# Kernel tuning notes

Measured on AMD Instinct MI355X. Metric: run time of the kernel, lower is better.

The kernel has to match this reference:

```python
import jax, jax.numpy as jnp
import numpy as np

ALPHA = 1.0

def setup_inputs() -> dict:
    key = jax.random.key(0)
    kz, kc = jax.random.split(key)
    N, K, D = 65536, 256, 256
    z = jax.random.normal(kz, (N, D), dtype=jnp.float32)
    centroids = jax.random.normal(kc, (K, D), dtype=jnp.float32)
    return {"z": z, "centroids": centroids}

def reference(z, centroids):
    # squared euclidean distances (N, K) via expansion; same math as
    # sum((z[:,None,:]-c)**2, -1) without the (N,K,D) intermediate
    z2 = jnp.sum(z * z, axis=1, keepdims=True)            # (N, 1)
    c2 = jnp.sum(centroids * centroids, axis=1)           # (K,)
    sse = jnp.maximum(z2 + c2[None, :] - 2.0 * (z @ centroids.T), 0.0)
    # Student-t kernel
    q = (1.0 + sse / ALPHA) ** (-(ALPHA + 1.0) / 2.0)
    q = q / jnp.sum(q, axis=1, keepdims=True)             # row normalize
    # target distribution p
    sf = q * q / jnp.sum(q, axis=0, keepdims=True)        # col normalize of q^2
    p = sf / jnp.sum(sf, axis=1, keepdims=True)           # row normalize
    return (p, q)
```

## Files before the change

kernel.cpp:

```cpp
#include <hip/hip_runtime.h>
#include <stdint.h>

#define N_ROWS 65536
#define K_CENT 256
#define D_DIM  256

typedef __attribute__((ext_vector_type(8))) short bf16x8;
typedef __attribute__((ext_vector_type(4))) float f32x4;

__device__ __forceinline__ float bf2f(unsigned short u) {
    union { unsigned int i; float f; } v;
    v.i = ((unsigned int)u) << 16;
    return v.f;
}

__device__ __forceinline__ unsigned short f2bf(float f) {
    union { float f; unsigned int i; } v;
    v.f = f;
    unsigned int r = (v.i + 0x7FFFu + ((v.i >> 16) & 1u)) >> 16;
    return (unsigned short)r;
}

__global__ void c2_kernel(const float* __restrict__ cent,
                          float* __restrict__ c2,
                          unsigned short* __restrict__ cent_bf) {
    int row  = blockIdx.x;
    int lane = threadIdx.x;
    const float4 v = *(const float4*)(cent + (size_t)row * D_DIM + lane * 4);
    unsigned short b0 = f2bf(v.x), b1 = f2bf(v.y), b2 = f2bf(v.z), b3 = f2bf(v.w);
    ushort4 bv; bv.x = b0; bv.y = b1; bv.z = b2; bv.w = b3;
    int blk = lane >> 1;
    int pos = row * D_DIM + (((blk ^ (row & 7)) << 3) | ((lane & 1) << 2));
    *(ushort4*)(cent_bf + pos) = bv;
    float f0 = bf2f(b0), f1 = bf2f(b1), f2 = bf2f(b2), f3 = bf2f(b3);
    float s = f0 * f0 + f1 * f1 + f2 * f2 + f3 * f3;
    #pragma unroll
    for (int off = 32; off >= 1; off >>= 1) s += __shfl_xor(s, off, 64);
    if (lane == 0) c2[row] = s;
}

__global__ __launch_bounds__(256, 3) void pass1_kernel(
        const float* __restrict__ z,
        const unsigned short* __restrict__ cent_bf,
        const float* __restrict__ c2,
        float* __restrict__ partials,
        float* __restrict__ q_out) {
    __shared__ __align__(16) unsigned short bstage[64 * D_DIM];
    __shared__ float col_lds[4][K_CENT];

    const int tid  = threadIdx.x;
    const int wave = tid >> 6;
    const int lane = tid & 63;
    const int m15  = lane & 15;
    const int quad = lane >> 4;
    const int row0 = blockIdx.x * 64 + wave * 16;

    const float* za = z + (size_t)(row0 + m15) * D_DIM + quad * 8;
    bf16x8 afrag[8];
    float z2p = 0.0f;
    #pragma unroll
    for (int h = 0; h < 2; ++h) {
        float4 a[8];
        #pragma unroll
        for (int i = 0; i < 4; ++i) {
            a[2 * i]     = *(const float4*)(za + h * 128 + i * 32);
            a[2 * i + 1] = *(const float4*)(za + h * 128 + i * 32 + 4);
        }
        #pragma unroll
        for (int i = 0; i < 4; ++i) {
            const int ks = h * 4 + i;
            const float av[8] = {a[2*i].x, a[2*i].y, a[2*i].z, a[2*i].w,
                                 a[2*i+1].x, a[2*i+1].y, a[2*i+1].z, a[2*i+1].w};
            #pragma unroll
            for (int j = 0; j < 8; ++j) {
                unsigned short ub = f2bf(av[j]);
                afrag[ks][j] = (short)ub;
                float f = bf2f(ub);
                z2p += f * f;
            }
        }
    }
    z2p += __shfl_xor(z2p, 16, 64);
    z2p += __shfl_xor(z2p, 32, 64);
    float z2r[4];
    #pragma unroll
    for (int r = 0; r < 4; ++r) z2r[r] = __shfl(z2p, quad * 4 + r, 64);

    f32x4 acc[16];
    #pragma unroll
    for (int t = 0; t < 16; ++t) acc[t] = (f32x4){0.f, 0.f, 0.f, 0.f};

    #pragma unroll
    for (int c = 0; c < 4; ++c) {
        const unsigned short* src = cent_bf + (size_t)c * 64 * D_DIM;
        bf16x8 st[8];
        #pragma unroll
        for (int i = 0; i < 8; ++i)
            st[i] = *(const bf16x8*)&src[(i * 256 + tid) * 8];
        #pragma unroll
        for (int i = 0; i < 8; ++i)
            *(bf16x8*)&bstage[(i * 256 + tid) * 8] = st[i];
        __syncthreads();
        #pragma unroll
        for (int ks = 0; ks < 8; ++ks) {
            #pragma unroll
            for (int t = 0; t < 4; ++t) {
                int r_local = t * 16 + m15;
                int b = quad + ks * 4;
                int pos = r_local * D_DIM + ((b ^ (r_local & 7)) << 3);
                bf16x8 bfrag = *(const bf16x8*)&bstage[pos];
                acc[c * 4 + t] = __builtin_amdgcn_mfma_f32_16x16x32_bf16(
                    afrag[ks], bfrag, acc[c * 4 + t], 0, 0, 0);
            }
        }
        __syncthreads();
    }

    float rowsum[4] = {0.f, 0.f, 0.f, 0.f};
    #pragma unroll
    for (int t = 0; t < 16; ++t) {
        float c2v = c2[t * 16 + m15];
        #pragma unroll
        for (int r = 0; r < 4; ++r) {
            float sse = z2r[r] + c2v - 2.0f * acc[t][r];
            sse = fmaxf(sse, 0.0f);
            float u = 1.0f / (1.0f + sse);
            acc[t][r] = u;
            rowsum[r] += u;
        }
    }
    #pragma unroll
    for (int r = 0; r < 4; ++r) {
        float v = rowsum[r];
        v += __shfl_xor(v, 1, 64);
        v += __shfl_xor(v, 2, 64);
        v += __shfl_xor(v, 4, 64);
        v += __shfl_xor(v, 8, 64);
        rowsum[r] = 1.0f / v;
    }

    float colp[16];
    #pragma unroll
    for (int t = 0; t < 16; ++t) {
        float cp = 0.0f;
        #pragma unroll
        for (int r = 0; r < 4; ++r) {
            float qv = acc[t][r] * rowsum[r];
            cp += qv;
            q_out[(size_t)(row0 + quad * 4 + r) * K_CENT + t * 16 + m15] = qv;
        }
        cp += __shfl_xor(cp, 16, 64);
        cp += __shfl_xor(cp, 32, 64);
        colp[t] = cp;
    }
    if (quad == 0) {
        #pragma unroll
        for (int t = 0; t < 16; ++t) col_lds[wave][t * 16 + lane] = colp[t];
    }
    __syncthreads();
    float sp = col_lds[0][tid] + col_lds[1][tid] + col_lds[2][tid] + col_lds[3][tid];
    partials[(size_t)blockIdx.x * K_CENT + tid] = sp;
}

__global__ __launch_bounds__(256) void colsum_kernel(
        const float* __restrict__ partials,
        float* __restrict__ s_col) {
    const int tid = threadIdx.x;
    const float* base = partials + (size_t)blockIdx.x * 64 * K_CENT + tid;
    float s = 0.0f;
    #pragma unroll
    for (int h = 0; h < 8; ++h) {
        float v[8];
        #pragma unroll
        for (int i = 0; i < 8; ++i)
            v[i] = base[(h * 8 + i) * K_CENT];
        #pragma unroll
        for (int i = 0; i < 8; ++i) s += v[i];
    }
    atomicAdd(&s_col[tid], s);
}

__global__ __launch_bounds__(256) void pass2_kernel(
        const float* __restrict__ q,
        const float* __restrict__ s_col,
        float* __restrict__ p) {
    const int tid  = threadIdx.x;
    const int lane = tid & 63;
    const int wave = tid >> 6;
    const int wid  = blockIdx.x * 4 + wave;

    const float4 sv = *(const float4*)(s_col + lane * 4);
    const float is0 = 1.0f / sv.x, is1 = 1.0f / sv.y,
                is2 = 1.0f / sv.z, is3 = 1.0f / sv.w;

    const float* qb = q + (size_t)wid * 8 * K_CENT + lane * 4;
    float*       pb = p + (size_t)wid * 8 * K_CENT + lane * 4;

    float4 qv[8];
    #pragma unroll
    for (int r = 0; r < 8; ++r) qv[r] = *(const float4*)(qb + r * K_CENT);

    #pragma unroll
    for (int r = 0; r < 8; ++r) {
        float sf0 = qv[r].x * qv[r].x * is0;
        float sf1 = qv[r].y * qv[r].y * is1;
        float sf2 = qv[r].z * qv[r].z * is2;
        float sf3 = qv[r].w * qv[r].w * is3;
        float part = sf0 + sf1 + sf2 + sf3;
        #pragma unroll
        for (int off = 32; off >= 1; off >>= 1) part += __shfl_xor(part, off, 64);
        const float rinv = 1.0f / part;
        float4 ov;
        ov.x = sf0 * rinv; ov.y = sf1 * rinv;
        ov.z = sf2 * rinv; ov.w = sf3 * rinv;
        *(float4*)(pb + r * K_CENT) = ov;
    }
}

extern "C" void kernel_launch(void* const* d_in, const int* in_sizes, int n_in,
                              void* d_out, int out_size, void* d_ws, size_t ws_size,
                              hipStream_t stream) {
    const float* z    = (const float*)d_in[0];
    const float* cent = (const float*)d_in[1];
    float* p_out = (float*)d_out;
    float* q_out = p_out + (size_t)N_ROWS * K_CENT;

    float* c2       = (float*)d_ws;
    float* s_col    = c2 + K_CENT;
    unsigned short* cent_bf = (unsigned short*)(s_col + K_CENT);
    float* partials = (float*)(cent_bf + K_CENT * D_DIM);

    hipMemsetAsync(s_col, 0, K_CENT * sizeof(float), stream);
    c2_kernel<<<K_CENT, 64, 0, stream>>>(cent, c2, cent_bf);
    pass1_kernel<<<N_ROWS / 64, 256, 0, stream>>>(z, cent_bf, c2, partials, q_out);
    colsum_kernel<<<16, 256, 0, stream>>>(partials, s_col);
    pass2_kernel<<<N_ROWS / (4 * 8), 256, 0, stream>>>(q_out, s_col, p_out);
}
```

Before: 219.7 us.

## Store centroids row-major and permute into fragment-ordered LDS layout during staging

The XOR-swizzled global layout of the bf16 centroids is replaced by plain row-major, and the staging loop now gathers global chunks so LDS holds B fragments in exact MFMA consumption order, making fragment reads linear and conflict-free. All z loads are issued up front in one batch instead of two halves, and the launch bound is raised to four blocks per CU. The gathered global reads are less coalesced and the extra in-flight loads and occupancy target may cause register pressure or spills.

New measurement: 212.4 us. -3.3%, faster.

```diff
diff --git a/kernel.cpp b/kernel.cpp
--- a/kernel.cpp
+++ b/kernel.cpp
@@ -29,9 +29,7 @@
     const float4 v = *(const float4*)(cent + (size_t)row * D_DIM + lane * 4);
     unsigned short b0 = f2bf(v.x), b1 = f2bf(v.y), b2 = f2bf(v.z), b3 = f2bf(v.w);
     ushort4 bv; bv.x = b0; bv.y = b1; bv.z = b2; bv.w = b3;
-    int blk = lane >> 1;
-    int pos = row * D_DIM + (((blk ^ (row & 7)) << 3) | ((lane & 1) << 2));
-    *(ushort4*)(cent_bf + pos) = bv;
+    *(ushort4*)(cent_bf + (size_t)row * D_DIM + lane * 4) = bv;
     float f0 = bf2f(b0), f1 = bf2f(b1), f2 = bf2f(b2), f3 = bf2f(b3);
     float s = f0 * f0 + f1 * f1 + f2 * f2 + f3 * f3;
     #pragma unroll
@@ -39,7 +37,7 @@
     if (lane == 0) c2[row] = s;
 }
 
-__global__ __launch_bounds__(256, 3) void pass1_kernel(
+__global__ __launch_bounds__(256, 4) void pass1_kernel(
         const float* __restrict__ z,
         const unsigned short* __restrict__ cent_bf,
         const float* __restrict__ c2,
@@ -56,28 +54,24 @@
     const int row0 = blockIdx.x * 64 + wave * 16;
 
     const float* za = z + (size_t)(row0 + m15) * D_DIM + quad * 8;
+    float4 a[16];
+    #pragma unroll
+    for (int i = 0; i < 8; ++i) {
+        a[2 * i]     = *(const float4*)(za + i * 32);
+        a[2 * i + 1] = *(const float4*)(za + i * 32 + 4);
+    }
     bf16x8 afrag[8];
     float z2p = 0.0f;
     #pragma unroll
-    for (int h = 0; h < 2; ++h) {
-        float4 a[8];
-        #pragma unroll
-        for (int i = 0; i < 4; ++i) {
-            a[2 * i]     = *(const float4*)(za + h * 128 + i * 32);
-            a[2 * i + 1] = *(const float4*)(za + h * 128 + i * 32 + 4);
-        }
-        #pragma unroll
-        for (int i = 0; i < 4; ++i) {
-            const int ks = h * 4 + i;
-            const float av[8] = {a[2*i].x, a[2*i].y, a[2*i].z, a[2*i].w,
-                                 a[2*i+1].x, a[2*i+1].y, a[2*i+1].z, a[2*i+1].w};
-            #pragma unroll
-            for (int j = 0; j < 8; ++j) {
-                unsigned short ub = f2bf(av[j]);
-                afrag[ks][j] = (short)ub;
-                float f = bf2f(ub);
-                z2p += f * f;
-            }
+    for (int ks = 0; ks < 8; ++ks) {
+        const float av[8] = {a[2*ks].x, a[2*ks].y, a[2*ks].z, a[2*ks].w,
+                             a[2*ks+1].x, a[2*ks+1].y, a[2*ks+1].z, a[2*ks+1].w};
+        #pragma unroll
+        for (int j = 0; j < 8; ++j) {
+            unsigned short ub = f2bf(av[j]);
+            afrag[ks][j] = (short)ub;
+            float f = bf2f(ub);
+            z2p += f * f;
         }
     }
     z2p += __shfl_xor(z2p, 16, 64);
@@ -93,22 +87,28 @@
     #pragma unroll
     for (int c = 0; c < 4; ++c) {
         const unsigned short* src = cent_bf + (size_t)c * 64 * D_DIM;
-        bf16x8 st[8];
-        #pragma unroll
-        for (int i = 0; i < 8; ++i)
-            st[i] = *(const bf16x8*)&src[(i * 256 + tid) * 8];
-        #pragma unroll
-        for (int i = 0; i < 8; ++i)
-            *(bf16x8*)&bstage[(i * 256 + tid) * 8] = st[i];
+        #pragma unroll
+        for (int h = 0; h < 2; ++h) {
+            bf16x8 st[4];
+            #pragma unroll
+            for (int i = 0; i < 4; ++i) {
+                int F  = (h * 4 + i) * 256 + tid;
+                int qd = F & 3, mm = (F >> 2) & 15, tt = (F >> 6) & 3, kk = F >> 8;
+                int s16 = tt * 512 + mm * 32 + kk * 4 + qd;
+                st[i] = *(const bf16x8*)&src[s16 * 8];
+            }
+            #pragma unroll
+            for (int i = 0; i < 4; ++i) {
+                int F = (h * 4 + i) * 256 + tid;
+                *(bf16x8*)&bstage[F * 8] = st[i];
+            }
+        }
         __syncthreads();
         #pragma unroll
         for (int ks = 0; ks < 8; ++ks) {
             #pragma unroll
             for (int t = 0; t < 4; ++t) {
-                int r_local = t * 16 + m15;
-                int b = quad + ks * 4;
-                int pos = r_local * D_DIM + ((b ^ (r_local & 7)) << 3);
-                bf16x8 bfrag = *(const bf16x8*)&bstage[pos];
+                bf16x8 bfrag = *(const bf16x8*)&bstage[(ks * 256 + t * 64 + m15 * 4 + quad) * 8];
                 acc[c * 4 + t] = __builtin_amdgcn_mfma_f32_16x16x32_bf16(
                     afrag[ks], bfrag, acc[c * 4 + t], 0, 0, 0);
             }
```
